# Kernel tuning notes

Measured on AMD Instinct MI355X. Metric: run time of the kernel, lower is better.

Reference implementation:

```python
import jax, jax.numpy as jnp
import numpy as np

NUM_CLASSES = 100000
NUM_SAMPLED = 5000  # num_classes * cr, cr = 0.05
BATCH = 4096
DIM = 1024


def _log_expected_count(idx, num_sampled, num_classes):
    # TF LogUniformCandidateSampler: P(c) = log((c+2)/(c+1)) / log(num_classes+1)
    c = idx.astype(jnp.float32)
    p = jnp.log((c + 2.0) / (c + 1.0)) / jnp.log(float(num_classes) + 1.0)
    # expected count for unique sampling of num_sampled candidates
    return jnp.log(-jnp.expm1(num_sampled * jnp.log1p(-p)))


def setup_inputs() -> dict:
    key = jax.random.key(0)
    k1, k2, k3, k4 = jax.random.split(key, 4)
    x = jax.random.normal(k1, (BATCH, DIM), dtype=jnp.float32)
    w = jax.random.normal(k2, (DIM, NUM_CLASSES), dtype=jnp.float32) * 0.05  # tf random_normal_initializer stddev
    b = jnp.zeros((NUM_CLASSES,), dtype=jnp.float32)
    labels = jax.random.randint(k3, (BATCH,), 0, NUM_CLASSES)
    sampled = jax.random.randint(k4, (NUM_SAMPLED,), 0, NUM_CLASSES)
    return {"x": x, "w": w, "b": b, "labels": labels, "sampled": sampled}


def reference(x, w, b, labels, sampled):
    # sampled-class logits: gather columns of w then one small GEMM
    w_s = w[:, sampled]                                   # [D, S]
    sampled_logits = x @ w_s + b[sampled][None, :]        # [B, S]
    sampled_logits = sampled_logits - _log_expected_count(sampled, NUM_SAMPLED, NUM_CLASSES)[None, :]
    # true-class logit per example
    w_t = w[:, labels]                                    # [D, B]
    true_logits = jnp.einsum('bd,db->b', x, w_t) + b[labels]
    true_logits = true_logits - _log_expected_count(labels, NUM_SAMPLED, NUM_CLASSES)
    # softmax CE with true class in column 0 of [true | sampled]
    all_logits = jnp.concatenate([true_logits[:, None], sampled_logits], axis=1)  # [B, 1+S]
    loss = jnp.mean(jax.nn.logsumexp(all_logits, axis=1) - true_logits)
    return loss
```

## Files before the change

kernel.cpp:

```cpp
#include <hip/hip_runtime.h>
#include <hip/hip_bf16.h>

#define NUM_CLASSES 100000
#define NUM_SAMPLED 5000
#define BATCH 4096
#define DIM 1024
#define NPAD 5120
#define NLINES 6250
#define SLACK 32

typedef float floatx4 __attribute__((ext_vector_type(4)));
typedef short bf16x8 __attribute__((ext_vector_type(8)));

__device__ __forceinline__ float log_expected_count(int c) {
    float p = log1pf(1.0f / (float)(c + 1)) / logf((float)NUM_CLASSES + 1.0f);
    float t = (float)NUM_SAMPLED * log1pf(-p);
    return logf(-expm1f(t));
}

__device__ __forceinline__ void async_ld16(const void* g, void* l) {
    __builtin_amdgcn_global_load_lds(
        (const __attribute__((address_space(1))) unsigned int*)g,
        (__attribute__((address_space(3))) unsigned int*)l,
        16, 0, 0);
}

__global__ __launch_bounds__(256) void setup_kernel(int* __restrict__ cnt,
                                                    float* __restrict__ rowsum,
                                                    uint4* __restrict__ btpad) {
    int i = blockIdx.x * 256 + threadIdx.x;
    if (i < NLINES) cnt[i] = 0;
    if (i < BATCH) rowsum[i] = 0.0f;
    if (i < (NPAD - NUM_SAMPLED) * DIM * 2 / 16) {
        uint4 z; z.x = z.y = z.z = z.w = 0u;
        btpad[i] = z;
    }
}

__global__ __launch_bounds__(256) void convert_x_kernel(const float* __restrict__ x,
                                                        __hip_bfloat16* __restrict__ A) {
    int i = (blockIdx.x * 256 + threadIdx.x) * 4;
    float4 v = *reinterpret_cast<const float4*>(x + i);
    union { ushort4 u; __hip_bfloat16 h[4]; } o;
    o.h[0] = __float2bfloat16(v.x);
    o.h[1] = __float2bfloat16(v.y);
    o.h[2] = __float2bfloat16(v.z);
    o.h[3] = __float2bfloat16(v.w);
    *reinterpret_cast<ushort4*>(A + i) = o.u;
}

__global__ __launch_bounds__(256) void bucket_kernel(const int* __restrict__ sampled,
                                                     const int* __restrict__ labels,
                                                     const float* __restrict__ b,
                                                     int* __restrict__ cnt,
                                                     unsigned* __restrict__ entries,
                                                     float* __restrict__ shift,
                                                     float* __restrict__ tlshift) {
    int t = blockIdx.x * 256 + threadIdx.x;
    if (t < NUM_SAMPLED) {
        int c = sampled[t];
        int pos = atomicAdd(&cnt[c >> 4], 1);
        if (pos < SLACK)
            entries[(c >> 4) * SLACK + pos] = ((unsigned)(c & 15) << 28) | (unsigned)t;
        shift[t] = b[c] - log_expected_count(c);
    } else if (t < NPAD) {
        shift[t] = -1e30f;
    } else if (t < NPAD + BATCH) {
        int m = t - NPAD;
        int c = labels[m];
        int pos = atomicAdd(&cnt[c >> 4], 1);
        if (pos < SLACK)
            entries[(c >> 4) * SLACK + pos] = ((unsigned)(c & 15) << 28) | (1u << 27) | (unsigned)m;
        tlshift[m] = b[c] - log_expected_count(c);
    }
}

__global__ __launch_bounds__(256) void extract_kernel(const float* __restrict__ w,
                                                      const int* __restrict__ cnt,
                                                      const unsigned* __restrict__ entries,
                                                      __hip_bfloat16* __restrict__ BT,
                                                      float* __restrict__ WT) {
    int line = blockIdx.x * 256 + threadIdx.x;
    int d = blockIdx.y;
    if (line >= NLINES) return;
    int c = cnt[line];
    if (c == 0) return;
    if (c > SLACK) c = SLACK;
    const float* src = w + (size_t)d * NUM_CLASSES + line * 16;
    for (int e = 0; e < c; e++) {
        unsigned E = entries[line * SLACK + e];
        float v = src[E >> 28];
        unsigned idx = E & 0x3FFFu;
        if (E & (1u << 27)) WT[(size_t)idx * DIM + d] = v;
        else                BT[(size_t)idx * DIM + d] = __float2bfloat16(v);
    }
}

#define BM 128
#define BN 128
#define BK 64

__global__ __launch_bounds__(256) void gemm_kernel(const __hip_bfloat16* __restrict__ A,
                                                   const __hip_bfloat16* __restrict__ BT,
                                                   const float* __restrict__ shift,
                                                   float* __restrict__ rowsum) {
    __shared__ __hip_bfloat16 As[BM * BK];
    __shared__ __hip_bfloat16 Bs[BN * BK];

    const int tid  = threadIdx.x;
    const int m0   = blockIdx.x * BM;
    const int n0   = blockIdx.y * BN;
    const int lane = tid & 63;
    const int wv   = tid >> 6;
    const int wm   = (wv >> 1) * 64;
    const int wn   = (wv & 1) * 64;
    const int col  = lane & 15;
    const int quad = lane >> 4;

    floatx4 acc[4][4] = {};

    const __hip_bfloat16* gA[4];
    const __hip_bfloat16* gB[4];
    int ldsOff[4];
    #pragma unroll
    for (int r = 0; r < 4; r++) {
        int eo  = tid * 8 + r * 2048;
        int row = eo >> 6;
        int cl  = eo & 63;
        gA[r] = A  + (size_t)(m0 + row) * DIM + cl;
        gB[r] = BT + (size_t)(n0 + row) * DIM + cl;
        ldsOff[r] = eo;
    }

    for (int kt = 0; kt < DIM; kt += BK) {
        #pragma unroll
        for (int r = 0; r < 4; r++)
            async_ld16(gA[r] + kt, &As[ldsOff[r]]);
        #pragma unroll
        for (int r = 0; r < 4; r++)
            async_ld16(gB[r] + kt, &Bs[ldsOff[r]]);
        __syncthreads();

        #pragma unroll
        for (int ks = 0; ks < 2; ks++) {
            const int kc = ks * 32 + quad * 8;
            bf16x8 af[4], bfr[4];
            #pragma unroll
            for (int i = 0; i < 4; i++) {
                af[i]  = *reinterpret_cast<const bf16x8*>(&As[(wm + i * 16 + col) * BK + kc]);
                bfr[i] = *reinterpret_cast<const bf16x8*>(&Bs[(wn + i * 16 + col) * BK + kc]);
            }
            #pragma unroll
            for (int i = 0; i < 4; i++)
                #pragma unroll
                for (int j = 0; j < 4; j++)
                    acc[i][j] = __builtin_amdgcn_mfma_f32_16x16x32_bf16(af[i], bfr[j], acc[i][j], 0, 0, 0);
        }
        __syncthreads();
    }

    float sh[4];
    #pragma unroll
    for (int j = 0; j < 4; j++)
        sh[j] = shift[n0 + wn + j * 16 + col];

    #pragma unroll
    for (int i = 0; i < 4; i++) {
        #pragma unroll
        for (int r = 0; r < 4; r++) {
            float s = 0.0f;
            #pragma unroll
            for (int j = 0; j < 4; j++)
                s += __expf(acc[i][j][r] + sh[j]);
            s += __shfl_xor(s, 1);
            s += __shfl_xor(s, 2);
            s += __shfl_xor(s, 4);
            s += __shfl_xor(s, 8);
            if (col == 0) {
                int mrow = m0 + wm + i * 16 + quad * 4 + r;
                atomicAdd(&rowsum[mrow], s);
            }
        }
    }
}

__global__ __launch_bounds__(256) void rowloss_kernel(const float* __restrict__ x,
                                                      const float* __restrict__ WT,
                                                      const float* __restrict__ tlshift,
                                                      const float* __restrict__ rowsum,
                                                      float* __restrict__ rowloss) {
    int m = blockIdx.x * 4 + (threadIdx.x >> 6);
    int lane = threadIdx.x & 63;
    const float4* xr = reinterpret_cast<const float4*>(x + (size_t)m * DIM);
    const float4* wr = reinterpret_cast<const float4*>(WT + (size_t)m * DIM);
    float p = 0.0f;
    #pragma unroll
    for (int j = 0; j < 4; j++) {
        float4 a = xr[lane + 64 * j];
        float4 b = wr[lane + 64 * j];
        p += a.x * b.x + a.y * b.y + a.z * b.z + a.w * b.w;
    }
    #pragma unroll
    for (int off = 32; off > 0; off >>= 1)
        p += __shfl_xor(p, off);
    if (lane == 0) {
        float tl = p + tlshift[m];
        float total = rowsum[m] + __expf(tl);
        rowloss[m] = logf(total) - tl;
    }
}

__global__ __launch_bounds__(256) void reduce_kernel(const float* __restrict__ rowloss,
                                                     float* __restrict__ out) {
    __shared__ float red[4];
    const int t = threadIdx.x;
    float s = 0.0f;
    #pragma unroll
    for (int i = t; i < BATCH; i += 256)
        s += rowloss[i];
    #pragma unroll
    for (int off = 32; off > 0; off >>= 1)
        s += __shfl_xor(s, off);
    if ((t & 63) == 0) red[t >> 6] = s;
    __syncthreads();
    if (t == 0)
        out[0] = (red[0] + red[1] + red[2] + red[3]) * (1.0f / (float)BATCH);
}

extern "C" void kernel_launch(void* const* d_in, const int* in_sizes, int n_in,
                              void* d_out, int out_size, void* d_ws, size_t ws_size,
                              hipStream_t stream) {
    const float* x       = (const float*)d_in[0];
    const float* w       = (const float*)d_in[1];
    const float* b       = (const float*)d_in[2];
    const int*   labels  = (const int*)d_in[3];
    const int*   sampled = (const int*)d_in[4];
    float* out = (float*)d_out;

    char* ws = (char*)d_ws;
    __hip_bfloat16* A  = (__hip_bfloat16*)(ws);
    __hip_bfloat16* BT = (__hip_bfloat16*)(ws + (size_t)8  * 1024 * 1024);
    float* WT      = (float*)(ws + (size_t)18 * 1024 * 1024);
    float* shift   = (float*)(ws + (size_t)34 * 1024 * 1024);
    float* tlshift = (float*)(ws + (size_t)34 * 1024 * 1024 + 64  * 1024);
    float* rowsum  = (float*)(ws + (size_t)34 * 1024 * 1024 + 128 * 1024);
    float* rowloss = (float*)(ws + (size_t)34 * 1024 * 1024 + 192 * 1024);
    int* cnt       = (int*)  (ws + (size_t)34 * 1024 * 1024 + 256 * 1024);
    unsigned* ent  = (unsigned*)(ws + (size_t)34 * 1024 * 1024 + 320 * 1024);

    hipLaunchKernelGGL(setup_kernel, dim3(64), dim3(256), 0, stream,
                       cnt, rowsum, (uint4*)(BT + (size_t)NUM_SAMPLED * DIM));
    hipLaunchKernelGGL(convert_x_kernel, dim3((BATCH * DIM / 4) / 256), dim3(256), 0, stream, x, A);
    hipLaunchKernelGGL(bucket_kernel, dim3((NPAD + BATCH) / 256), dim3(256), 0, stream,
                       sampled, labels, b, cnt, ent, shift, tlshift);
    hipLaunchKernelGGL(extract_kernel, dim3((NLINES + 255) / 256, DIM), dim3(256), 0, stream,
                       w, cnt, ent, BT, WT);
    hipLaunchKernelGGL(gemm_kernel, dim3(BATCH / BM, NPAD / BN), dim3(256), 0, stream,
                       A, BT, shift, rowsum);
    hipLaunchKernelGGL(rowloss_kernel, dim3(BATCH / 4), dim3(256), 0, stream,
                       x, WT, tlshift, rowsum, rowloss);
    hipLaunchKernelGGL(reduce_kernel, dim3(1), dim3(256), 0, stream, rowloss, out);
}
```

Before: 735.3 us.

## Restructure column extraction with shared-memory staging and vectorized row writes

The extract kernel now tiles 64 cache lines by 32 feature rows per block. It first builds a per-block list of needed columns in shared memory, then gathers w values into an LDS tile and writes 8 consecutive d values per store, as float4 pairs or bf16x8. The old version wrote one scalar per thread at stride DIM, which scattered the writes into BT/WT. This trades those strided scalar stores for contiguous vector stores, but adds block syncs and a list cap of 512 entries per block that could drop entries if exceeded.

```diff
diff --git a/kernel.cpp b/kernel.cpp
--- a/kernel.cpp
+++ b/kernel.cpp
@@ -75,24 +75,85 @@
     }
 }
 
+#define LPB 64
+#define DPB 32
+#define ECHUNK 128
+#define LISTCAP 512
+
 __global__ __launch_bounds__(256) void extract_kernel(const float* __restrict__ w,
                                                       const int* __restrict__ cnt,
                                                       const unsigned* __restrict__ entries,
                                                       __hip_bfloat16* __restrict__ BT,
                                                       float* __restrict__ WT) {
-    int line = blockIdx.x * 256 + threadIdx.x;
-    int d = blockIdx.y;
-    if (line >= NLINES) return;
-    int c = cnt[line];
-    if (c == 0) return;
-    if (c > SLACK) c = SLACK;
-    const float* src = w + (size_t)d * NUM_CLASSES + line * 16;
-    for (int e = 0; e < c; e++) {
-        unsigned E = entries[line * SLACK + e];
-        float v = src[E >> 28];
-        unsigned idx = E & 0x3FFFu;
-        if (E & (1u << 27)) WT[(size_t)idx * DIM + d] = v;
-        else                BT[(size_t)idx * DIM + d] = __float2bfloat16(v);
+    __shared__ float val[DPB][ECHUNK];
+    __shared__ unsigned list[LISTCAP];
+    __shared__ int ecount;
+
+    const int tid = threadIdx.x;
+    const int L0  = blockIdx.x * LPB;
+    const int d0  = blockIdx.y * DPB;
+    const int C0  = L0 * 16;
+
+    if (tid == 0) ecount = 0;
+    __syncthreads();
+
+    if (tid < LPB) {
+        int line = L0 + tid;
+        if (line < NLINES) {
+            int c = cnt[line];
+            if (c > SLACK) c = SLACK;
+            for (int e = 0; e < c; e++) {
+                unsigned E = entries[line * SLACK + e];
+                int pos = atomicAdd(&ecount, 1);
+                if (pos < LISTCAP)
+                    list[pos] = ((unsigned)(tid * 16 + (E >> 28)) << 16)
+                              | (((E >> 27) & 1u) << 15)
+                              | (E & 0x3FFFu);
+            }
+        }
+    }
+    __syncthreads();
+    int E_blk = ecount;
+    if (E_blk > LISTCAP) E_blk = LISTCAP;
+    if (E_blk == 0) return;
+
+    for (int base = 0; base < E_blk; base += ECHUNK) {
+        int Ec = E_blk - base;
+        if (Ec > ECHUNK) Ec = ECHUNK;
+
+        for (int i = tid; i < DPB * ECHUNK; i += 256) {
+            int e  = i & (ECHUNK - 1);
+            int dj = i >> 7;
+            if (e < Ec) {
+                unsigned L = list[base + e];
+                int cl = L >> 16;
+                val[dj][e] = w[(size_t)(d0 + dj) * NUM_CLASSES + C0 + cl];
+            }
+        }
+        __syncthreads();
+
+        for (int i = tid; i < 4 * ECHUNK; i += 256) {
+            int e  = i & (ECHUNK - 1);
+            int ch = i >> 7;
+            if (e < Ec) {
+                unsigned L = list[base + e];
+                unsigned idx = L & 0x7FFFu;
+                int dj = ch * 8;
+                if (L & (1u << 15)) {
+                    float4 a = { val[dj+0][e], val[dj+1][e], val[dj+2][e], val[dj+3][e] };
+                    float4 c = { val[dj+4][e], val[dj+5][e], val[dj+6][e], val[dj+7][e] };
+                    float4* dst = reinterpret_cast<float4*>(WT + (size_t)idx * DIM + d0 + dj);
+                    dst[0] = a; dst[1] = c;
+                } else {
+                    union { uint4 u; __hip_bfloat16 h[8]; } o;
+                    #pragma unroll
+                    for (int j = 0; j < 8; j++)
+                        o.h[j] = __float2bfloat16(val[dj + j][e]);
+                    *reinterpret_cast<uint4*>(BT + (size_t)idx * DIM + d0 + dj) = o.u;
+                }
+            }
+        }
+        __syncthreads();
     }
 }
 
@@ -253,7 +314,7 @@
     hipLaunchKernelGGL(convert_x_kernel, dim3((BATCH * DIM / 4) / 256), dim3(256), 0, stream, x, A);
     hipLaunchKernelGGL(bucket_kernel, dim3((NPAD + BATCH) / 256), dim3(256), 0, stream,
                        sampled, labels, b, cnt, ent, shift, tlshift);
-    hipLaunchKernelGGL(extract_kernel, dim3((NLINES + 255) / 256, DIM), dim3(256), 0, stream,
+    hipLaunchKernelGGL(extract_kernel, dim3((NLINES + LPB - 1) / LPB, DIM / DPB), dim3(256), 0, stream,
                        w, cnt, ent, BT, WT);
     hipLaunchKernelGGL(gemm_kernel, dim3(BATCH / BM, NPAD / BN), dim3(256), 0, stream,
                        A, BT, shift, rowsum);
```

Result: faster. 659.0 us (-10.4%).
